# Optimization experiments

Hardware: AMD Instinct MI355X
Metric: run time of the kernel (lower is better)

## Reference

```python
import jax, jax.numpy as jnp
import numpy as np

NX, NU, ND = 512, 128, 64
BATCH, T = 256, 256


def setup_inputs() -> dict:
    key = jax.random.key(0)
    ks = jax.random.split(key, 7)
    return {
        "x": jax.random.normal(ks[0], (BATCH, NX), dtype=jnp.float32),
        "U": jax.random.normal(ks[1], (T, BATCH, NU), dtype=jnp.float32),
        "D": jax.random.normal(ks[2], (T, BATCH, ND), dtype=jnp.float32),
        "A_weight": jax.random.normal(ks[3], (NX, NX), dtype=jnp.float32),
        "A_scalar": jax.random.normal(ks[4], (NX, NX), dtype=jnp.float32),
        "B_weight": jax.random.normal(ks[5], (NX, NU), dtype=jnp.float32) * 0.05,
        "E_weight": jax.random.normal(ks[6], (NX, ND), dtype=jnp.float32) * 0.05,
    }


def _effective_W(weight, scalar):
    # (1 - 0.1*sigmoid(scalar)) * softmax(weight, axis=1), then transposed
    s_clamped = 1.0 - 0.1 * jax.nn.sigmoid(scalar)
    return (s_clamped * jax.nn.softmax(weight, axis=1)).T  # [nx, nx]


def reference(x, U, D, A_weight, A_scalar, B_weight, E_weight):
    W_eff = _effective_W(A_weight, A_scalar)            # hoisted: constant over time
    # Precompute input injections: [T, batch, nx]
    inj = jnp.einsum('tbu,xu->tbx', U, B_weight) + jnp.einsum('tbd,xd->tbx', D, E_weight)

    def step(x_prev, inj_t):
        x_new = x_prev @ W_eff + inj_t
        return x_new, x_new

    _, X = jax.lax.scan(step, x, inj)                   # X: [T, batch, nx]
    Y = X[:, :, -1]                                     # [T, batch]
    return X, Y
```

## Files before the change

### kernel.cpp

```cpp
#include <hip/hip_runtime.h>
#include <hip/hip_bf16.h>
#include <cstddef>

#define NXX 512
#define NUU 128
#define NDD 64
#define BB  256
#define TT  256
#define CL  8
#define NC  32
#define BS  (BB * NXX)
#define MS  (NXX * NXX)
#define LDK 32

typedef __attribute__((ext_vector_type(8))) short short8;
typedef __attribute__((ext_vector_type(8))) unsigned short ushort8;
typedef __attribute__((ext_vector_type(4))) unsigned short ushort4v;
typedef __attribute__((ext_vector_type(4))) float f32x4;

__device__ __forceinline__ unsigned short f2bf(float f) {
    union { float f; unsigned u; } v; v.f = f;
    unsigned r = v.u + 0x7FFFu + ((v.u >> 16) & 1u);
    return (unsigned short)(r >> 16);
}
__device__ __forceinline__ float bf2f(unsigned short h) {
    union { unsigned u; float f; } v; v.u = ((unsigned)h) << 16;
    return v.f;
}

enum StageKind { SK_BF16_NAT, SK_BF16_TRANS };

__device__ __forceinline__ void stage_nat(const unsigned short* s, int ld, int r0,
                                          int k0, unsigned short (*S)[LDK])
{
    const int tid = threadIdx.x;
    const int wave = tid >> 6, lane = tid & 63;
#pragma unroll
    for (int i = 0; i < 2; ++i) {
        int rb = wave * 16 + i * 64;
        int r  = rb + (lane >> 2);
        int c  = (lane & 3) << 3;
        const unsigned short* g = s + (size_t)(r0 + r) * ld + k0 + c;
        __builtin_amdgcn_global_load_lds(
            (const __attribute__((address_space(1))) void*)g,
            (__attribute__((address_space(3))) void*)&S[rb][0],
            16, 0, 0);
    }
}
__device__ __forceinline__ ushort8 ldT(const unsigned short* s, int ld, int r0,
                                       int k0, int i)
{
    int idx = threadIdx.x + i * 256;
    int m   = idx >> 4;
    int c   = (idx & 15) << 3;
    return *(const ushort8*)(s + (size_t)(k0 + m) * ld + r0 + c);
}
__device__ __forceinline__ void wrT(ushort8 v, int i, unsigned short (*S)[LDK])
{
    int idx = threadIdx.x + i * 256;
    int m   = idx >> 4;
    int c   = (idx & 15) << 3;
#pragma unroll
    for (int j = 0; j < 8; ++j) S[c + j][m] = v[j];
}

template<StageKind AK, StageKind BK>
__device__ __forceinline__ void gemm2_mainloop(
    f32x4 (&acc)[4][4],
    const void* A, int lda, const void* B, int ldb,
    int K, int row0, int n0,
    unsigned short (*As)[128][LDK], unsigned short (*Bs)[128][LDK])
{
    const int tid  = threadIdx.x;
    const int lane = tid & 63;
    const int wave = tid >> 6;
    const int wm   = (wave >> 1) * 64;
    const int wn   = (wave & 1) * 64;
    const int l16  = lane & 15;
    const int quad = lane >> 4;
    const unsigned short* Ap = (const unsigned short*)A;
    const unsigned short* Bp = (const unsigned short*)B;
    const int NT = K >> 5;

    if constexpr (AK == SK_BF16_NAT) stage_nat(Ap, lda, row0, 0, As[0]);
    else { wrT(ldT(Ap, lda, row0, 0, 0), 0, As[0]); wrT(ldT(Ap, lda, row0, 0, 1), 1, As[0]); }
    if constexpr (BK == SK_BF16_NAT) stage_nat(Bp, ldb, n0, 0, Bs[0]);
    else { wrT(ldT(Bp, ldb, n0, 0, 0), 0, Bs[0]); wrT(ldT(Bp, ldb, n0, 0, 1), 1, Bs[0]); }
    __syncthreads();

    for (int t = 0; t < NT; ++t) {
        const int cur = t & 1, nxt = cur ^ 1;
        const int k1  = (t + 1) << 5;
        ushort8 ta0, ta1, tb0, tb1;
        if (t + 1 < NT) {
            if constexpr (AK == SK_BF16_NAT) stage_nat(Ap, lda, row0, k1, As[nxt]);
            else { ta0 = ldT(Ap, lda, row0, k1, 0); ta1 = ldT(Ap, lda, row0, k1, 1); }
            if constexpr (BK == SK_BF16_NAT) stage_nat(Bp, ldb, n0, k1, Bs[nxt]);
            else { tb0 = ldT(Bp, ldb, n0, k1, 0); tb1 = ldT(Bp, ldb, n0, k1, 1); }
        }
        short8 af[4], bfr[4];
#pragma unroll
        for (int f = 0; f < 4; ++f)
            af[f] = *(const short8*)&As[cur][wm + f * 16 + l16][quad * 8];
#pragma unroll
        for (int f = 0; f < 4; ++f)
            bfr[f] = *(const short8*)&Bs[cur][wn + f * 16 + l16][quad * 8];
#pragma unroll
        for (int fm = 0; fm < 4; ++fm)
#pragma unroll
            for (int fn = 0; fn < 4; ++fn)
                acc[fm][fn] = __builtin_amdgcn_mfma_f32_16x16x32_bf16(
                    af[fm], bfr[fn], acc[fm][fn], 0, 0, 0);
        if (t + 1 < NT) {
            if constexpr (AK == SK_BF16_TRANS) { wrT(ta0, 0, As[nxt]); wrT(ta1, 1, As[nxt]); }
            if constexpr (BK == SK_BF16_TRANS) { wrT(tb0, 0, Bs[nxt]); wrT(tb1, 1, Bs[nxt]); }
        }
        __syncthreads();
    }
}

__global__ __launch_bounds__(256) void k_weff(
    const float* __restrict__ Aw, const float* __restrict__ Asc,
    unsigned short* __restrict__ T1)
{
    const int n   = blockIdx.x;
    const int tid = threadIdx.x;
    const int lane = tid & 63, wave = tid >> 6;
    float v0 = Aw[(size_t)n * NXX + tid];
    float v1 = Aw[(size_t)n * NXX + 256 + tid];
    __shared__ float sred[4];
    float m = fmaxf(v0, v1);
#pragma unroll
    for (int off = 32; off; off >>= 1) m = fmaxf(m, __shfl_down(m, off));
    if (lane == 0) sred[wave] = m;
    __syncthreads();
    if (tid == 0) sred[0] = fmaxf(fmaxf(sred[0], sred[1]), fmaxf(sred[2], sred[3]));
    __syncthreads();
    const float mm = sred[0];
    __syncthreads();
    float e0 = expf(v0 - mm), e1 = expf(v1 - mm);
    float s = e0 + e1;
#pragma unroll
    for (int off = 32; off; off >>= 1) s += __shfl_down(s, off);
    if (lane == 0) sred[wave] = s;
    __syncthreads();
    if (tid == 0) sred[0] = sred[0] + sred[1] + sred[2] + sred[3];
    __syncthreads();
    const float inv = 1.0f / sred[0];
    float sc0 = 1.0f - 0.1f * (1.0f / (1.0f + expf(-Asc[(size_t)n * NXX + tid])));
    float sc1 = 1.0f - 0.1f * (1.0f / (1.0f + expf(-Asc[(size_t)n * NXX + 256 + tid])));
    unsigned short* out = T1 + (size_t)n * NXX;
    out[tid]       = f2bf(sc0 * e0 * inv);
    out[tid + 256] = f2bf(sc1 * e1 * inv);
}

__global__ __launch_bounds__(256) void k_prep(
    const float* __restrict__ Bw, const float* __restrict__ Ew,
    const float* __restrict__ x,
    unsigned short* __restrict__ Bwb, unsigned short* __restrict__ Ewb,
    unsigned short* __restrict__ G0)
{
    int i = (blockIdx.x * 256 + threadIdx.x) * 4;
    const float* src; unsigned short* dst; int k;
    if (i < 65536)       { src = Bw; dst = Bwb; k = i; }
    else if (i < 98304)  { src = Ew; dst = Ewb; k = i - 65536; }
    else                 { src = x;  dst = G0;  k = i - 98304; }
    float4 v = *(const float4*)(src + k);
    ushort4v h = { f2bf(v.x), f2bf(v.y), f2bf(v.z), f2bf(v.w) };
    *(ushort4v*)(dst + k) = h;
}

__global__ __launch_bounds__(256) void k_mulN(unsigned short* __restrict__ powb,
                                              int4 ns, int4 ts, int4 ds)
{
    const int z = blockIdx.z;
    const int an = (z == 0) ? ns.x : (z == 1) ? ns.y : (z == 2) ? ns.z : ns.w;
    const int at = (z == 0) ? ts.x : (z == 1) ? ts.y : (z == 2) ? ts.z : ts.w;
    const int ad = (z == 0) ? ds.x : (z == 1) ? ds.y : (z == 2) ? ds.z : ds.w;
    const unsigned short* A = powb + (size_t)an * MS;
    const unsigned short* B = powb + (size_t)at * MS;
    unsigned short*       D = powb + (size_t)ad * MS;
    __shared__ unsigned short As[2][128][LDK];
    __shared__ unsigned short Bs2[2][128][LDK];
    f32x4 acc[4][4] = {};
    const int row0 = blockIdx.y * 128, n0 = blockIdx.x * 128;
    gemm2_mainloop<SK_BF16_NAT, SK_BF16_TRANS>(acc, A, NXX, B, NXX, NXX, row0, n0, As, Bs2);
    const int tid = threadIdx.x;
    const int lane = tid & 63, wave = tid >> 6;
    const int wm = (wave >> 1) * 64, wn = (wave & 1) * 64;
    const int l16 = lane & 15, quad = lane >> 4;
#pragma unroll
    for (int fm = 0; fm < 4; ++fm)
#pragma unroll
        for (int fn = 0; fn < 4; ++fn)
#pragma unroll
            for (int r = 0; r < 4; ++r) {
                int m = row0 + wm + fm * 16 + quad * 4 + r;
                int n = n0 + wn + fn * 16 + l16;
                D[(size_t)m * NXX + n] = f2bf(acc[fm][fn][r]);
            }
}

__global__ __launch_bounds__(256) void k_hs_sq(
    const unsigned short* __restrict__ vsrc, unsigned short* __restrict__ vdst,
    const unsigned short* __restrict__ Am, int s,
    unsigned short* __restrict__ powb, int sqa, int sqd)
{
    const int z = blockIdx.z;
    const int tid = threadIdx.x;
    __shared__ unsigned short As[2][128][LDK];
    __shared__ unsigned short Bs2[2][128][LDK];
    const int lane = tid & 63, wave = tid >> 6;
    const int wm = (wave >> 1) * 64, wn = (wave & 1) * 64;
    const int l16 = lane & 15, quad = lane >> 4;

    if (z >= NC) {
        const unsigned short* Aq = powb + (size_t)sqa * MS;
        unsigned short*       Dq = powb + (size_t)sqd * MS;
        const int row0 = (blockIdx.y + 2 * (z - NC)) * 128;
        const int n0   = blockIdx.x * 128;
        f32x4 acc[4][4] = {};
        gemm2_mainloop<SK_BF16_NAT, SK_BF16_TRANS>(acc, Aq, NXX, Aq, NXX, NXX, row0, n0, As, Bs2);
#pragma unroll
        for (int fm = 0; fm < 4; ++fm)
#pragma unroll
            for (int fn = 0; fn < 4; ++fn)
#pragma unroll
                for (int r = 0; r < 4; ++r) {
                    int m = row0 + wm + fm * 16 + quad * 4 + r;
                    int n = n0 + wn + fn * 16 + l16;
                    Dq[(size_t)m * NXX + n] = f2bf(acc[fm][fn][r]);
                }
        return;
    }

    const int c = z;
    const int row0 = blockIdx.y * 128, n0 = blockIdx.x * 128;
    if (c < s) {
        const unsigned short* sp = vsrc + (size_t)c * BS;
        unsigned short*       dp = vdst + (size_t)c * BS;
#pragma unroll
        for (int i = 0; i < 8; ++i) {
            int idx = tid + i * 256;
            int r = idx >> 4, cc = (idx & 15) << 3;
            *(ushort8*)(dp + (size_t)(row0 + r) * NXX + n0 + cc) =
                *(const ushort8*)(sp + (size_t)(row0 + r) * NXX + n0 + cc);
        }
        return;
    }
    f32x4 acc[4][4] = {};
    gemm2_mainloop<SK_BF16_NAT, SK_BF16_NAT>(acc, vsrc + (size_t)(c - s) * BS, NXX,
                                             Am, NXX, NXX, row0, n0, As, Bs2);
    const unsigned short* Cp = vsrc + (size_t)c * BS;
    unsigned short*       Dp = vdst + (size_t)c * BS;
#pragma unroll
    for (int fm = 0; fm < 4; ++fm)
#pragma unroll
        for (int fn = 0; fn < 4; ++fn)
#pragma unroll
            for (int r = 0; r < 4; ++r) {
                int m = row0 + wm + fm * 16 + quad * 4 + r;
                int n = n0 + wn + fn * 16 + l16;
                float v = acc[fm][fn][r] + bf2f(Cp[(size_t)m * NXX + n]);
                Dp[(size_t)m * NXX + n] = f2bf(v);
            }
}

__global__ __launch_bounds__(256) void k_xcorr(
    const unsigned short* __restrict__ vA, const unsigned short* __restrict__ powb,
    float* __restrict__ X, float* __restrict__ Y)
{
    const int t = blockIdx.z;
    const int c = t >> 3, j = t & 7;
    const int row0 = blockIdx.y * 128, n0 = blockIdx.x * 128;
    __shared__ unsigned short As[2][128][LDK];
    __shared__ unsigned short Bs2[2][128][LDK];
    f32x4 acc[4][4] = {};
    gemm2_mainloop<SK_BF16_NAT, SK_BF16_NAT>(acc, vA + (size_t)c * BS, NXX,
                                             powb + (size_t)j * MS, NXX, NXX,
                                             row0, n0, As, Bs2);
    const int tid = threadIdx.x;
    const int lane = tid & 63, wave = tid >> 6;
    const int wm = (wave >> 1) * 64, wn = (wave & 1) * 64;
    const int l16 = lane & 15, quad = lane >> 4;
    float* Xt = X + (size_t)t * BB * NXX;
#pragma unroll
    for (int fm = 0; fm < 4; ++fm)
#pragma unroll
        for (int fn = 0; fn < 4; ++fn)
#pragma unroll
            for (int r = 0; r < 4; ++r) {
                int m = row0 + wm + fm * 16 + quad * 4 + r;
                int n = n0 + wn + fn * 16 + l16;
                float v = acc[fm][fn][r] + Xt[(size_t)m * NXX + n];
                Xt[(size_t)m * NXX + n] = v;
                if (n == NXX - 1) Y[(size_t)t * BB + m] = v;
            }
}

__global__ __launch_bounds__(1024, 4) void k_scanA(
    const float* __restrict__ U, const float* __restrict__ Dm,
    const unsigned short* __restrict__ Bwb, const unsigned short* __restrict__ Ewb,
    const unsigned short* __restrict__ Wt,
    unsigned short* __restrict__ Gout,
    float* __restrict__ X)
{
    const int c   = blockIdx.x;
    const int r0  = blockIdx.y * 32;
    const int tid = threadIdx.x;
    const int lane = tid & 63, wave = tid >> 6;
    const int l16 = lane & 15, quad = lane >> 4;

    __shared__ unsigned short Sb[2][32][520];
    __shared__ unsigned short Ub[2][32][136];
    __shared__ unsigned short Db[2][32][72];

    const int srow = tid >> 5;
    const int su   = (tid & 31) * 4;
    const int sd   = (tid & 31) * 2;

    {
        const float* up = U + ((size_t)(c * CL) * BB + r0 + srow) * NUU + su;
        float4 a0 = *(const float4*)up;
        ushort4v h0 = { f2bf(a0.x), f2bf(a0.y), f2bf(a0.z), f2bf(a0.w) };
        *(ushort4v*)&Ub[0][srow][su] = h0;
        const float* dp = Dm + ((size_t)(c * CL) * BB + r0 + srow) * NDD + sd;
        float2 b0 = *(const float2*)dp;
        unsigned pk = (unsigned)f2bf(b0.x) | ((unsigned)f2bf(b0.y) << 16);
        *(unsigned*)&Db[0][srow][sd] = pk;
    }

    int woff[2], bwoff[2], ewoff[2];
#pragma unroll
    for (int g = 0; g < 2; ++g) {
        int n = wave * 32 + g * 16 + l16;
        woff[g]  = n * NXX + quad * 8;
        bwoff[g] = n * NUU + quad * 8;
        ewoff[g] = n * NDD + quad * 8;
    }

    f32x4 acc[2][2];

    for (int j = 0; j < CL; ++j) {
        const int t   = c * CL + j;
        const int cur = j & 1, nxt = cur ^ 1;

        __syncthreads();

        float4 pu; float2 pd;
        if (j + 1 < CL) {
            pu = *(const float4*)(U + ((size_t)(t + 1) * BB + r0 + srow) * NUU + su);
            pd = *(const float2*)(Dm + ((size_t)(t + 1) * BB + r0 + srow) * NDD + sd);
        }

#pragma unroll
        for (int f = 0; f < 2; ++f)
#pragma unroll
            for (int g = 0; g < 2; ++g) acc[f][g] = (f32x4){0.f, 0.f, 0.f, 0.f};

#pragma unroll
        for (int kk = 0; kk < 4; ++kk) {
            short8 a0 = *(const short8*)&Ub[cur][l16][kk * 32 + quad * 8];
            short8 a1 = *(const short8*)&Ub[cur][16 + l16][kk * 32 + quad * 8];
#pragma unroll
            for (int g = 0; g < 2; ++g) {
                short8 b = *(const short8*)(Bwb + bwoff[g] + kk * 32);
                acc[0][g] = __builtin_amdgcn_mfma_f32_16x16x32_bf16(a0, b, acc[0][g], 0, 0, 0);
                acc[1][g] = __builtin_amdgcn_mfma_f32_16x16x32_bf16(a1, b, acc[1][g], 0, 0, 0);
            }
        }
#pragma unroll
        for (int kk = 0; kk < 2; ++kk) {
            short8 a0 = *(const short8*)&Db[cur][l16][kk * 32 + quad * 8];
            short8 a1 = *(const short8*)&Db[cur][16 + l16][kk * 32 + quad * 8];
#pragma unroll
            for (int g = 0; g < 2; ++g) {
                short8 b = *(const short8*)(Ewb + ewoff[g] + kk * 32);
                acc[0][g] = __builtin_amdgcn_mfma_f32_16x16x32_bf16(a0, b, acc[0][g], 0, 0, 0);
                acc[1][g] = __builtin_amdgcn_mfma_f32_16x16x32_bf16(a1, b, acc[1][g], 0, 0, 0);
            }
        }
        if (j > 0) {
#pragma unroll
            for (int kk = 0; kk < 16; ++kk) {
                short8 a0 = *(const short8*)&Sb[cur][l16][kk * 32 + quad * 8];
                short8 a1 = *(const short8*)&Sb[cur][16 + l16][kk * 32 + quad * 8];
#pragma unroll
                for (int g = 0; g < 2; ++g) {
                    short8 b = *(const short8*)(Wt + woff[g] + kk * 32);
                    acc[0][g] = __builtin_amdgcn_mfma_f32_16x16x32_bf16(a0, b, acc[0][g], 0, 0, 0);
                    acc[1][g] = __builtin_amdgcn_mfma_f32_16x16x32_bf16(a1, b, acc[1][g], 0, 0, 0);
                }
            }
        }

#pragma unroll
        for (int f = 0; f < 2; ++f)
#pragma unroll
            for (int g = 0; g < 2; ++g) {
                int n = wave * 32 + g * 16 + l16;
#pragma unroll
                for (int rr = 0; rr < 4; ++rr) {
                    int mr = f * 16 + quad * 4 + rr;
                    float v = acc[f][g][rr];
                    unsigned short hb = f2bf(v);
                    Sb[nxt][mr][n] = hb;
                    X[((size_t)t * BB + r0 + mr) * NXX + n] = v;
                    if (j == CL - 1)
                        Gout[((size_t)(c + 1) * BB + r0 + mr) * NXX + n] = hb;
                }
            }

        if (j + 1 < CL) {
            ushort4v h0 = { f2bf(pu.x), f2bf(pu.y), f2bf(pu.z), f2bf(pu.w) };
            *(ushort4v*)&Ub[nxt][srow][su] = h0;
            unsigned pk = (unsigned)f2bf(pd.x) | ((unsigned)f2bf(pd.y) << 16);
            *(unsigned*)&Db[nxt][srow][sd] = pk;
        }
    }
}

extern "C" void kernel_launch(void* const* d_in, const int* in_sizes, int n_in,
                              void* d_out, int out_size, void* d_ws, size_t ws_size,
                              hipStream_t stream)
{
    const float* x   = (const float*)d_in[0];
    const float* U   = (const float*)d_in[1];
    const float* Dm  = (const float*)d_in[2];
    const float* Aw  = (const float*)d_in[3];
    const float* Asc = (const float*)d_in[4];
    const float* Bw  = (const float*)d_in[5];
    const float* Ew  = (const float*)d_in[6];

    float* Xout = (float*)d_out;
    float* Yout = Xout + (size_t)TT * BB * NXX;

    unsigned short* powb = (unsigned short*)d_ws;
    unsigned short* Bwb  = powb + (size_t)12 * MS;
    unsigned short* Ewb  = Bwb + (size_t)NXX * NUU;
    unsigned short* Gbuf = Ewb + (size_t)NXX * NDD;
    unsigned short* vA   = Gbuf + (size_t)(NC + 1) * BS;
    unsigned short* vB   = vA + (size_t)NC * BS;

    dim3 blk(256);
    dim3 blkScan(1024);

    k_weff<<<dim3(512), blk, 0, stream>>>(Aw, Asc, powb);
    k_prep<<<dim3(224), blk, 0, stream>>>(Bw, Ew, x, Bwb, Ewb, Gbuf);

    k_mulN<<<dim3(4, 4, 1), blk, 0, stream>>>(powb,
        make_int4(0, 0, 0, 0), make_int4(0, 0, 0, 0), make_int4(1, 0, 0, 0));
    k_mulN<<<dim3(4, 4, 2), blk, 0, stream>>>(powb,
        make_int4(1, 1, 0, 0), make_int4(0, 1, 0, 0), make_int4(2, 3, 0, 0));
    k_mulN<<<dim3(4, 4, 4), blk, 0, stream>>>(powb,
        make_int4(3, 3, 3, 3), make_int4(0, 1, 2, 3), make_int4(4, 5, 6, 7));

    k_scanA<<<dim3(NC, 8), blkScan, 0, stream>>>(
        U, Dm, Bwb, Ewb, powb, Gbuf, Xout);

    k_hs_sq<<<dim3(4, 2, NC + 2), blk, 0, stream>>>(Gbuf, vA, powb + (size_t)7 * MS, 1,
                                                    powb, 7, 8);
    k_hs_sq<<<dim3(4, 2, NC + 2), blk, 0, stream>>>(vA, vB, powb + (size_t)8 * MS, 2,
                                                    powb, 8, 9);
    k_hs_sq<<<dim3(4, 2, NC + 2), blk, 0, stream>>>(vB, vA, powb + (size_t)9 * MS, 4,
                                                    powb, 9, 10);
    k_hs_sq<<<dim3(4, 2, NC + 2), blk, 0, stream>>>(vA, vB, powb + (size_t)10 * MS, 8,
                                                    powb, 10, 11);
    k_hs_sq<<<dim3(4, 2, NC), blk, 0, stream>>>(vB, vA, powb + (size_t)11 * MS, 16,
                                                powb, 0, 0);

    k_xcorr<<<dim3(4, 2, TT), blk, 0, stream>>>(vA, powb, Xout, Yout);
}
```

Before: 611.4 us.

## Halve scan chunk length to double chunks, add extra doubling pass

Chunk length drops from 8 to 4 steps, so there are 64 chunks and the sequential per-chunk scan gets shorter and runs more blocks in parallel. The chain of matrix powers is cut down (only W^1..W^3 are precomputed for in-chunk use) while the Hillis-Steele carry propagation gains a sixth squaring pass over twice as many chunk seeds. The scan kernel also drops its double-buffered LDS prefetch of U/D in favour of single buffers with an extra barrier, which cuts LDS use so more blocks fit per CU. The cost is more carry-propagation GEMM work across more chunks and lost overlap of input loads inside the scan.

```diff
diff --git a/kernel.cpp b/kernel.cpp
--- a/kernel.cpp
+++ b/kernel.cpp
@@ -7,8 +7,8 @@
 #define NDD 64
 #define BB  256
 #define TT  256
-#define CL  8
-#define NC  32
+#define CL  4
+#define NC  64
 #define BS  (BB * NXX)
 #define MS  (NXX * NXX)
 #define LDK 32
@@ -267,16 +267,16 @@
 }
 
 __global__ __launch_bounds__(256) void k_xcorr(
-    const unsigned short* __restrict__ vA, const unsigned short* __restrict__ powb,
+    const unsigned short* __restrict__ seeds, const unsigned short* __restrict__ powb,
     float* __restrict__ X, float* __restrict__ Y)
 {
     const int t = blockIdx.z;
-    const int c = t >> 3, j = t & 7;
+    const int c = t >> 2, j = t & 3;
     const int row0 = blockIdx.y * 128, n0 = blockIdx.x * 128;
     __shared__ unsigned short As[2][128][LDK];
     __shared__ unsigned short Bs2[2][128][LDK];
     f32x4 acc[4][4] = {};
-    gemm2_mainloop<SK_BF16_NAT, SK_BF16_NAT>(acc, vA + (size_t)c * BS, NXX,
+    gemm2_mainloop<SK_BF16_NAT, SK_BF16_NAT>(acc, seeds + (size_t)c * BS, NXX,
                                              powb + (size_t)j * MS, NXX, NXX,
                                              row0, n0, As, Bs2);
     const int tid = threadIdx.x;
@@ -298,7 +298,7 @@
             }
 }
 
-__global__ __launch_bounds__(1024, 4) void k_scanA(
+__global__ __launch_bounds__(1024, 8) void k_scanA(
     const float* __restrict__ U, const float* __restrict__ Dm,
     const unsigned short* __restrict__ Bwb, const unsigned short* __restrict__ Ewb,
     const unsigned short* __restrict__ Wt,
@@ -311,24 +311,9 @@
     const int lane = tid & 63, wave = tid >> 6;
     const int l16 = lane & 15, quad = lane >> 4;
 
-    __shared__ unsigned short Sb[2][32][520];
-    __shared__ unsigned short Ub[2][32][136];
-    __shared__ unsigned short Db[2][32][72];
-
-    const int srow = tid >> 5;
-    const int su   = (tid & 31) * 4;
-    const int sd   = (tid & 31) * 2;
-
-    {
-        const float* up = U + ((size_t)(c * CL) * BB + r0 + srow) * NUU + su;
-        float4 a0 = *(const float4*)up;
-        ushort4v h0 = { f2bf(a0.x), f2bf(a0.y), f2bf(a0.z), f2bf(a0.w) };
-        *(ushort4v*)&Ub[0][srow][su] = h0;
-        const float* dp = Dm + ((size_t)(c * CL) * BB + r0 + srow) * NDD + sd;
-        float2 b0 = *(const float2*)dp;
-        unsigned pk = (unsigned)f2bf(b0.x) | ((unsigned)f2bf(b0.y) << 16);
-        *(unsigned*)&Db[0][srow][sd] = pk;
-    }
+    __shared__ unsigned short Sb[32][520];
+    __shared__ unsigned short Ub[32][136];
+    __shared__ unsigned short Db[32][72];
 
     int woff[2], bwoff[2], ewoff[2];
 #pragma unroll
@@ -342,17 +327,22 @@
     f32x4 acc[2][2];
 
     for (int j = 0; j < CL; ++j) {
-        const int t   = c * CL + j;
-        const int cur = j & 1, nxt = cur ^ 1;
-
+        const int t = c * CL + j;
+        {
+            int row = tid >> 5;
+            int uc  = (tid & 31) * 4;
+            const float* up = U + ((size_t)t * BB + r0 + row) * NUU + uc;
+            float4 a0 = *(const float4*)(up);
+            ushort4v h0 = { f2bf(a0.x), f2bf(a0.y), f2bf(a0.z), f2bf(a0.w) };
+            *(ushort4v*)&Ub[row][uc] = h0;
+            int dc = (tid & 31) * 2;
+            const float* dp = Dm + ((size_t)t * BB + r0 + row) * NDD + dc;
+            float2 b0 = *(const float2*)(dp);
+            unsigned pk = (unsigned)f2bf(b0.x) | ((unsigned)f2bf(b0.y) << 16);
+            *(unsigned*)&Db[row][dc] = pk;
+        }
         __syncthreads();
 
-        float4 pu; float2 pd;
-        if (j + 1 < CL) {
-            pu = *(const float4*)(U + ((size_t)(t + 1) * BB + r0 + srow) * NUU + su);
-            pd = *(const float2*)(Dm + ((size_t)(t + 1) * BB + r0 + srow) * NDD + sd);
-        }
-
 #pragma unroll
         for (int f = 0; f < 2; ++f)
 #pragma unroll
@@ -360,8 +350,8 @@
 
 #pragma unroll
         for (int kk = 0; kk < 4; ++kk) {
-            short8 a0 = *(const short8*)&Ub[cur][l16][kk * 32 + quad * 8];
-            short8 a1 = *(const short8*)&Ub[cur][16 + l16][kk * 32 + quad * 8];
+            short8 a0 = *(const short8*)&Ub[l16][kk * 32 + quad * 8];
+            short8 a1 = *(const short8*)&Ub[16 + l16][kk * 32 + quad * 8];
 #pragma unroll
             for (int g = 0; g < 2; ++g) {
                 short8 b = *(const short8*)(Bwb + bwoff[g] + kk * 32);
@@ -371,8 +361,8 @@
         }
 #pragma unroll
         for (int kk = 0; kk < 2; ++kk) {
-            short8 a0 = *(const short8*)&Db[cur][l16][kk * 32 + quad * 8];
-            short8 a1 = *(const short8*)&Db[cur][16 + l16][kk * 32 + quad * 8];
+            short8 a0 = *(const short8*)&Db[l16][kk * 32 + quad * 8];
+            short8 a1 = *(const short8*)&Db[16 + l16][kk * 32 + quad * 8];
 #pragma unroll
             for (int g = 0; g < 2; ++g) {
                 short8 b = *(const short8*)(Ewb + ewoff[g] + kk * 32);
@@ -383,8 +373,8 @@
         if (j > 0) {
 #pragma unroll
             for (int kk = 0; kk < 16; ++kk) {
-                short8 a0 = *(const short8*)&Sb[cur][l16][kk * 32 + quad * 8];
-                short8 a1 = *(const short8*)&Sb[cur][16 + l16][kk * 32 + quad * 8];
+                short8 a0 = *(const short8*)&Sb[l16][kk * 32 + quad * 8];
+                short8 a1 = *(const short8*)&Sb[16 + l16][kk * 32 + quad * 8];
 #pragma unroll
                 for (int g = 0; g < 2; ++g) {
                     short8 b = *(const short8*)(Wt + woff[g] + kk * 32);
@@ -393,6 +383,7 @@
                 }
             }
         }
+        __syncthreads();
 
 #pragma unroll
         for (int f = 0; f < 2; ++f)
@@ -404,19 +395,12 @@
                     int mr = f * 16 + quad * 4 + rr;
                     float v = acc[f][g][rr];
                     unsigned short hb = f2bf(v);
-                    Sb[nxt][mr][n] = hb;
+                    Sb[mr][n] = hb;
                     X[((size_t)t * BB + r0 + mr) * NXX + n] = v;
                     if (j == CL - 1)
                         Gout[((size_t)(c + 1) * BB + r0 + mr) * NXX + n] = hb;
                 }
             }
-
-        if (j + 1 < CL) {
-            ushort4v h0 = { f2bf(pu.x), f2bf(pu.y), f2bf(pu.z), f2bf(pu.w) };
-            *(ushort4v*)&Ub[nxt][srow][su] = h0;
-            unsigned pk = (unsigned)f2bf(pd.x) | ((unsigned)f2bf(pd.y) << 16);
-            *(unsigned*)&Db[nxt][srow][sd] = pk;
-        }
     }
 }
 
@@ -436,11 +420,10 @@
     float* Yout = Xout + (size_t)TT * BB * NXX;
 
     unsigned short* powb = (unsigned short*)d_ws;
-    unsigned short* Bwb  = powb + (size_t)12 * MS;
+    unsigned short* Bwb  = powb + (size_t)9 * MS;
     unsigned short* Ewb  = Bwb + (size_t)NXX * NUU;
     unsigned short* Gbuf = Ewb + (size_t)NXX * NDD;
     unsigned short* vA   = Gbuf + (size_t)(NC + 1) * BS;
-    unsigned short* vB   = vA + (size_t)NC * BS;
 
     dim3 blk(256);
     dim3 blkScan(1024);
@@ -452,22 +435,22 @@
         make_int4(0, 0, 0, 0), make_int4(0, 0, 0, 0), make_int4(1, 0, 0, 0));
     k_mulN<<<dim3(4, 4, 2), blk, 0, stream>>>(powb,
         make_int4(1, 1, 0, 0), make_int4(0, 1, 0, 0), make_int4(2, 3, 0, 0));
-    k_mulN<<<dim3(4, 4, 4), blk, 0, stream>>>(powb,
-        make_int4(3, 3, 3, 3), make_int4(0, 1, 2, 3), make_int4(4, 5, 6, 7));
 
     k_scanA<<<dim3(NC, 8), blkScan, 0, stream>>>(
         U, Dm, Bwb, Ewb, powb, Gbuf, Xout);
 
-    k_hs_sq<<<dim3(4, 2, NC + 2), blk, 0, stream>>>(Gbuf, vA, powb + (size_t)7 * MS, 1,
+    k_hs_sq<<<dim3(4, 2, NC + 2), blk, 0, stream>>>(Gbuf, vA, powb + (size_t)3 * MS, 1,
+                                                    powb, 3, 4);
+    k_hs_sq<<<dim3(4, 2, NC + 2), blk, 0, stream>>>(vA, Gbuf, powb + (size_t)4 * MS, 2,
+                                                    powb, 4, 5);
+    k_hs_sq<<<dim3(4, 2, NC + 2), blk, 0, stream>>>(Gbuf, vA, powb + (size_t)5 * MS, 4,
+                                                    powb, 5, 6);
+    k_hs_sq<<<dim3(4, 2, NC + 2), blk, 0, stream>>>(vA, Gbuf, powb + (size_t)6 * MS, 8,
+                                                    powb, 6, 7);
+    k_hs_sq<<<dim3(4, 2, NC + 2), blk, 0, stream>>>(Gbuf, vA, powb + (size_t)7 * MS, 16,
                                                     powb, 7, 8);
-    k_hs_sq<<<dim3(4, 2, NC + 2), blk, 0, stream>>>(vA, vB, powb + (size_t)8 * MS, 2,
-                                                    powb, 8, 9);
-    k_hs_sq<<<dim3(4, 2, NC + 2), blk, 0, stream>>>(vB, vA, powb + (size_t)9 * MS, 4,
-                                                    powb, 9, 10);
-    k_hs_sq<<<dim3(4, 2, NC + 2), blk, 0, stream>>>(vA, vB, powb + (size_t)10 * MS, 8,
-                                                    powb, 10, 11);
-    k_hs_sq<<<dim3(4, 2, NC), blk, 0, stream>>>(vB, vA, powb + (size_t)11 * MS, 16,
+    k_hs_sq<<<dim3(4, 2, NC), blk, 0, stream>>>(vA, Gbuf, powb + (size_t)8 * MS, 32,
                                                 powb, 0, 0);
 
-    k_xcorr<<<dim3(4, 2, TT), blk, 0, stream>>>(vA, powb, Xout, Yout);
-}
+    k_xcorr<<<dim3(4, 2, TT), blk, 0, stream>>>(Gbuf, powb, Xout, Yout);
+}
```

After: 654.6 us. 7.1% more time.
